# Optimization experiments

Measured on AMD Instinct MI355X. Metric: run time of the kernel, lower is better.

Reference implementation:

```python
import jax, jax.numpy as jnp
import numpy as np

N = 50000      # nodes
E = 800000     # edges
H = 4          # heads (all layers)
D = 64         # per-head out dim (n_hidden == n_classes == 64)
IN = 256       # in_feats; also H*D so identity residual is valid
NEG_SLOPE = 0.2


def setup_inputs() -> dict:
    key = jax.random.key(0)
    ks = jax.random.split(key, 16)
    x = jax.random.normal(ks[0], (N, IN), dtype=jnp.float32)
    src = jax.random.randint(ks[1], (E,), 0, N, dtype=jnp.int32)
    dst = jax.random.randint(ks[2], (E,), 0, N, dtype=jnp.int32)
    inp = {"x": x, "src": src, "dst": dst}
    fan_ins = [IN, H * D, H * D]  # layer input widths
    for i, fin in enumerate(fan_ins):
        s = 1.0 / np.sqrt(fin)
        inp[f"W{i}"] = jax.random.normal(ks[3 + 4 * i], (fin, H * D), dtype=jnp.float32) * s
        inp[f"al{i}"] = jax.random.normal(ks[4 + 4 * i], (H, D), dtype=jnp.float32) * s
        inp[f"ar{i}"] = jax.random.normal(ks[5 + 4 * i], (H, D), dtype=jnp.float32) * s
        inp[f"b{i}"] = jnp.zeros((H * D,), dtype=jnp.float32)
    return inp


def _gat_layer(h, src, dst, W, al, ar, b, residual, activate):
    # project: [N, in] @ [in, H*D] -> [N, H, D]
    feat = (h @ W).reshape(-1, H, D)
    el = jnp.sum(feat * al, axis=-1)            # [N, H]
    er = jnp.sum(feat * ar, axis=-1)            # [N, H]
    e = jax.nn.leaky_relu(el[src] + er[dst], NEG_SLOPE)  # [E, H]
    # edge softmax per destination node (stable: subtract per-dst max)
    emax = jax.ops.segment_max(e, dst, num_segments=N)  # [N, H]
    e = jnp.exp(e - emax[dst])
    denom = jax.ops.segment_sum(e, dst, num_segments=N)  # [N, H]
    alpha = e / denom[dst]                               # [E, H]
    # message + scatter-aggregate: [E, H, D] summed into [N, H, D]
    out = jax.ops.segment_sum(alpha[:, :, None] * feat[src], dst, num_segments=N)
    if residual:
        out = out + h.reshape(-1, H, D)  # identity residual (in == H*D)
    out = out + b.reshape(1, H, D)
    if activate:
        out = jax.nn.elu(out)
    return out


def reference(x, src, dst, W0, al0, ar0, b0, W1, al1, ar1, b1, W2, al2, ar2, b2):
    h = _gat_layer(x, src, dst, W0, al0, ar0, b0, False, True).reshape(N, H * D)
    h = _gat_layer(h, src, dst, W1, al1, ar1, b1, True, True).reshape(N, H * D)
    h = _gat_layer(h, src, dst, W2, al2, ar2, b2, True, False).mean(axis=1)  # [N, D]
    return h
```

## Files before the change

### kernel.cpp

```cpp
#include <hip/hip_runtime.h>
#include <math.h>

#define N_NODES 50000
#define N_EDGES 800000
#define HD 256
#define NHEAD 4
#define DH 64

typedef short bf16x8 __attribute__((ext_vector_type(8)));
typedef float f32x4 __attribute__((ext_vector_type(4)));

__device__ __forceinline__ unsigned short f2bf(float f) {
    unsigned u = __float_as_uint(f);
    return (unsigned short)((u + 0x7fffu + ((u >> 16) & 1u)) >> 16);
}
__device__ __forceinline__ float bf2f(unsigned short h) {
    return __uint_as_float((unsigned)h << 16);
}
__device__ __forceinline__ int origk(int k) {
    return (k & ~63) | ((k & 3) * 16 + ((k >> 2) & 15));
}

__global__ void packw_k(const float* __restrict__ W0, const float* __restrict__ W1,
                        const float* __restrict__ W2, unsigned short* __restrict__ Wp,
                        int* __restrict__ deg) {
    int blk = blockIdx.x;
    int L = blk >> 7, t = blk & 127;
    const float* W = L == 0 ? W0 : L == 1 ? W1 : W2;
    int nt = t >> 3, kt = t & 7;
    int lane = threadIdx.x;
    for (int i = blk * 64 + lane; i < N_NODES; i += 384 * 64) deg[i] = 0;
    int col = nt * 16 + (lane & 15);
    int kb = kt * 32 + (lane >> 4) * 8;
    unsigned short v[8];
#pragma unroll
    for (int j = 0; j < 8; j++) {
        int k = kb + j;
        if (L > 0) k = origk(k);
        v[j] = f2bf(W[(size_t)k * 256 + col]);
    }
    *(bf16x8*)(Wp + ((size_t)(L * 128 + t) * 64 + lane) * 8) = *(bf16x8*)v;
}

__device__ __forceinline__ void mfma_tile(const unsigned short* Asl,
                                          const unsigned short* wbase,
                                          int lane, f32x4 acc[4][4]) {
#pragma unroll
    for (int kk = 0; kk < 8; kk++) {
        bf16x8 a[4], b[4];
#pragma unroll
        for (int m = 0; m < 4; m++) {
            int r = m * 16 + (lane & 15);
            int kb = kk * 32 + (lane >> 4) * 8;
            int byt = (r * 512 + kb * 2) ^ ((r & 7) << 4);
            a[m] = *(const bf16x8*)((const char*)Asl + byt);
        }
#pragma unroll
        for (int n = 0; n < 4; n++)
            b[n] = *(const bf16x8*)(wbase + ((size_t)(n * 8 + kk) * 64 + lane) * 8);
#pragma unroll
        for (int m = 0; m < 4; m++)
#pragma unroll
            for (int n = 0; n < 4; n++)
                acc[m][n] = __builtin_amdgcn_mfma_f32_16x16x32_bf16(a[m], b[n],
                                                                    acc[m][n], 0, 0, 0);
    }
}

__device__ __forceinline__ void epilogue_tile(f32x4 acc[4][4], int bm, int wv, int lane,
                                              const float* __restrict__ al,
                                              const float* __restrict__ ar,
                                              unsigned short* __restrict__ C,
                                              float* __restrict__ el,
                                              float* __restrict__ er, int M) {
    int rr = lane >> 4, cc = lane & 15;
    float alv[4], arv[4];
#pragma unroll
    for (int n = 0; n < 4; n++) {
        alv[n] = al[wv * 64 + n * 16 + cc];
        arv[n] = ar[wv * 64 + n * 16 + cc];
    }
    float vl[16], vr[16];
#pragma unroll
    for (int m = 0; m < 4; m++)
#pragma unroll
        for (int r = 0; r < 4; r++) {
            float ep = 0.f, rp = 0.f;
#pragma unroll
            for (int n = 0; n < 4; n++) {
                ep = fmaf(acc[m][n][r], alv[n], ep);
                rp = fmaf(acc[m][n][r], arv[n], rp);
            }
            vl[m * 4 + r] = ep;
            vr[m * 4 + r] = rp;
        }
    float l8[8], r8[8];
#pragma unroll
    for (int i = 0; i < 8; i++) {
        float xs = (cc & 1) ? vl[2 * i] : vl[2 * i + 1];
        float xk = (cc & 1) ? vl[2 * i + 1] : vl[2 * i];
        l8[i] = xk + __shfl_xor(xs, 1);
        float ys = (cc & 1) ? vr[2 * i] : vr[2 * i + 1];
        float yk = (cc & 1) ? vr[2 * i + 1] : vr[2 * i];
        r8[i] = yk + __shfl_xor(ys, 1);
    }
    float l4[4], r4[4];
#pragma unroll
    for (int i = 0; i < 4; i++) {
        float xs = (cc & 2) ? l8[2 * i] : l8[2 * i + 1];
        float xk = (cc & 2) ? l8[2 * i + 1] : l8[2 * i];
        l4[i] = xk + __shfl_xor(xs, 2);
        float ys = (cc & 2) ? r8[2 * i] : r8[2 * i + 1];
        float yk = (cc & 2) ? r8[2 * i + 1] : r8[2 * i];
        r4[i] = yk + __shfl_xor(ys, 2);
    }
    float l2[2], r2[2];
#pragma unroll
    for (int i = 0; i < 2; i++) {
        float xs = (cc & 4) ? l4[2 * i] : l4[2 * i + 1];
        float xk = (cc & 4) ? l4[2 * i + 1] : l4[2 * i];
        l2[i] = xk + __shfl_xor(xs, 4);
        float ys = (cc & 4) ? r4[2 * i] : r4[2 * i + 1];
        float yk = (cc & 4) ? r4[2 * i + 1] : r4[2 * i];
        r2[i] = yk + __shfl_xor(ys, 4);
    }
    {
        float xs = (cc & 8) ? l2[0] : l2[1];
        float xk = (cc & 8) ? l2[1] : l2[0];
        float lv = xk + __shfl_xor(xs, 8);
        float ys = (cc & 8) ? r2[0] : r2[1];
        float yk = (cc & 8) ? r2[1] : r2[0];
        float rv = yk + __shfl_xor(ys, 8);
        int row_e = bm + (cc >> 2) * 16 + rr * 4 + (cc & 3);
        if (row_e < M) {
            el[(size_t)row_e * NHEAD + wv] = lv;
            er[(size_t)row_e * NHEAD + wv] = rv;
        }
    }
#pragma unroll
    for (int m = 0; m < 4; m++) {
#pragma unroll
        for (int r = 0; r < 4; r++) {
            int row = bm + m * 16 + rr * 4 + r;
            if (row < M) {
                unsigned short p4[4] = {f2bf(acc[m][0][r]), f2bf(acc[m][1][r]),
                                        f2bf(acc[m][2][r]), f2bf(acc[m][3][r])};
                *(ushort4*)(C + (size_t)row * 256 + wv * 64 + cc * 4) = *(ushort4*)p4;
            }
        }
    }
}

__global__ __launch_bounds__(256) void gemm0_k(const float* __restrict__ A,
                                               const unsigned short* __restrict__ Wp,
                                               const float* __restrict__ al,
                                               const float* __restrict__ ar,
                                               unsigned short* __restrict__ C,
                                               float* __restrict__ el,
                                               float* __restrict__ er, int M) {
    __shared__ unsigned short Asl[64 * 256];
    int tid = threadIdx.x, wv = tid >> 6, lane = tid & 63;
    int bm = blockIdx.x * 64;
#pragma unroll
    for (int i = 0; i < 8; i++) {
        int chunk = i * 256 + tid;
        int r = chunk >> 5, kc = (chunk & 31) * 8;
        float4 f0, f1;
        if (bm + r < M) {
            const float* p = A + (size_t)(bm + r) * 256 + kc;
            f0 = *(const float4*)p;
            f1 = *(const float4*)(p + 4);
        } else {
            f0 = f1 = make_float4(0.f, 0.f, 0.f, 0.f);
        }
        unsigned short tmp[8] = {f2bf(f0.x), f2bf(f0.y), f2bf(f0.z), f2bf(f0.w),
                                 f2bf(f1.x), f2bf(f1.y), f2bf(f1.z), f2bf(f1.w)};
        int b = (r * 512 + kc * 2) ^ ((r & 7) << 4);
        *(bf16x8*)((char*)Asl + b) = *(bf16x8*)tmp;
    }
    __syncthreads();
    const unsigned short* wbase = Wp + (size_t)(wv * 4) * 8 * 64 * 8;
    f32x4 acc[4][4] = {};
    mfma_tile(Asl, wbase, lane, acc);
    epilogue_tile(acc, bm, wv, lane, al, ar, C, el, er, M);
}

__global__ __launch_bounds__(256) void gemm2_k(const unsigned short* __restrict__ A,
                                               const unsigned short* __restrict__ Wp,
                                               const float* __restrict__ al,
                                               const float* __restrict__ ar,
                                               unsigned short* __restrict__ C,
                                               float* __restrict__ el,
                                               float* __restrict__ er, int M) {
    __shared__ unsigned short Asl[2][64 * 256];
    int tid = threadIdx.x, wv = tid >> 6, lane = tid & 63;
    int bm0 = blockIdx.x * 128, bm1 = bm0 + 64;
#pragma unroll
    for (int i = 0; i < 8; i++) {
        int chunk = i * 256 + tid;
        int r = chunk >> 5;
        int c16 = (chunk & 31) ^ (r & 7);
        int grow = bm0 + r; if (grow >= M) grow = M - 1;
        __builtin_amdgcn_global_load_lds(
            (const __attribute__((address_space(1))) unsigned int*)
                (A + (size_t)grow * 256 + c16 * 8),
            (__attribute__((address_space(3))) unsigned int*)
                ((char*)Asl[0] + (size_t)chunk * 16),
            16, 0, 0);
    }
#pragma unroll
    for (int i = 0; i < 8; i++) {
        int chunk = i * 256 + tid;
        int r = chunk >> 5;
        int c16 = (chunk & 31) ^ (r & 7);
        int grow = bm1 + r; if (grow >= M) grow = M - 1;
        __builtin_amdgcn_global_load_lds(
            (const __attribute__((address_space(1))) unsigned int*)
                (A + (size_t)grow * 256 + c16 * 8),
            (__attribute__((address_space(3))) unsigned int*)
                ((char*)Asl[1] + (size_t)chunk * 16),
            16, 0, 0);
    }
    asm volatile("s_waitcnt vmcnt(8)" ::: "memory");
    __builtin_amdgcn_sched_barrier(0);
    __builtin_amdgcn_s_barrier();
    const unsigned short* wbase = Wp + (size_t)(wv * 4) * 8 * 64 * 8;
    f32x4 acc[4][4] = {};
    mfma_tile(Asl[0], wbase, lane, acc);
    asm volatile("s_waitcnt vmcnt(0)" ::: "memory");
    __builtin_amdgcn_sched_barrier(0);
    __builtin_amdgcn_s_barrier();
    epilogue_tile(acc, bm0, wv, lane, al, ar, C, el, er, M);
    f32x4 acc2[4][4] = {};
    mfma_tile(Asl[1], wbase, lane, acc2);
    epilogue_tile(acc2, bm1, wv, lane, al, ar, C, el, er, M);
}

__global__ void hist_k(const int* __restrict__ dst, int* __restrict__ deg) {
    int e = (blockIdx.x * 256 + threadIdx.x) * 2;
    if (e + 1 < N_EDGES) {
        int2 d2 = *(const int2*)(dst + e);
        atomicAdd(&deg[d2.x], 1);
        atomicAdd(&deg[d2.y], 1);
    } else if (e < N_EDGES) {
        atomicAdd(&deg[dst[e]], 1);
    }
}

__global__ __launch_bounds__(1024) void scan1_k(const int* __restrict__ deg,
                                                int* __restrict__ rowptr,
                                                int* __restrict__ bsum) {
    __shared__ int wsum[16];
    int tid = threadIdx.x, lane = tid & 63, wv = tid >> 6;
    int i = blockIdx.x * 1024 + tid;
    int v = (i < N_NODES) ? deg[i] : 0;
    int sc = v;
#pragma unroll
    for (int o = 1; o < 64; o <<= 1) {
        int t = __shfl_up(sc, o);
        if (lane >= o) sc += t;
    }
    if (lane == 63) wsum[wv] = sc;
    __syncthreads();
    if (wv == 0 && lane < 16) {
        int ws = wsum[lane];
#pragma unroll
        for (int o = 1; o < 16; o <<= 1) {
            int t = __shfl_up(ws, o);
            if (lane >= o) ws += t;
        }
        wsum[lane] = ws;
    }
    __syncthreads();
    int incl = sc + (wv > 0 ? wsum[wv - 1] : 0);
    if (i < N_NODES) rowptr[i + 1] = incl;
    if (tid == 1023) bsum[blockIdx.x] = incl;
}

__global__ __launch_bounds__(1024) void scan3_k(int* __restrict__ rowptr,
                                                const int* __restrict__ bsum,
                                                int* __restrict__ cursor, int nb) {
    __shared__ int boff_s;
    int tid = threadIdx.x;
    if (tid < 64) {
        int v = (tid < nb) ? bsum[tid] : 0;
        int sc = v;
#pragma unroll
        for (int o = 1; o < 64; o <<= 1) {
            int t = __shfl_up(sc, o);
            if ((tid & 63) >= o) sc += t;
        }
        if (tid == (int)blockIdx.x) boff_s = sc - v;
    }
    __syncthreads();
    int off = boff_s;
    int i = blockIdx.x * 1024 + tid;
    if (blockIdx.x == 0 && tid == 0) { rowptr[0] = 0; cursor[0] = 0; }
    if (i < N_NODES) {
        int v = rowptr[i + 1] + off;
        rowptr[i + 1] = v;
        if (i + 1 < N_NODES) cursor[i + 1] = v;
    }
}

__global__ void scatter_k(const int* __restrict__ src, const int* __restrict__ dst,
                          int* __restrict__ cursor, int* __restrict__ csr_src) {
    int e = (blockIdx.x * 256 + threadIdx.x) * 2;
    if (e + 1 < N_EDGES) {
        int2 s2 = *(const int2*)(src + e);
        int2 d2 = *(const int2*)(dst + e);
        csr_src[atomicAdd(&cursor[d2.x], 1)] = s2.x;
        csr_src[atomicAdd(&cursor[d2.y], 1)] = s2.y;
    } else if (e < N_EDGES) {
        csr_src[atomicAdd(&cursor[dst[e]], 1)] = src[e];
    }
}

template <int MODE>
__global__ __launch_bounds__(256) void agg_k(const int* __restrict__ rowptr,
                                             const int* __restrict__ csr_src,
                                             const float* __restrict__ el,
                                             const float* __restrict__ er,
                                             const unsigned short* __restrict__ feat,
                                             const unsigned short* __restrict__ resid,
                                             const float* __restrict__ bias,
                                             float* __restrict__ out,
                                             unsigned short* __restrict__ hb) {
    __shared__ int   ws_s[4][64];
    __shared__ float ws_w[4][4][68];
    int wv = threadIdx.x >> 6, lane = threadIdx.x & 63;
    int node = blockIdx.x * 4 + wv;
    if (node >= N_NODES) return;
    int beg = rowptr[node], end = rowptr[node + 1];
    float4 er4 = *(const float4*)(er + (size_t)node * 4);
    float4 acc0 = make_float4(0.f, 0.f, 0.f, 0.f);
    float4 acc1 = make_float4(0.f, 0.f, 0.f, 0.f);
    float4 den = make_float4(0.f, 0.f, 0.f, 0.f);
    int h = lane >> 4;
    int l8 = lane * 8;
    const char* fb = (const char*)feat;
    for (int base = beg; base < end; base += 64) {
        int j = base + lane;
        int soff = 0;
        float4 w = make_float4(0.f, 0.f, 0.f, 0.f);
        if (j < end) {
            int s = csr_src[j];
            soff = s << 9;
            float4 l4 = *(const float4*)(el + (size_t)s * 4);
            float vx = l4.x + er4.x; vx = vx > 0.f ? vx : 0.2f * vx;
            float vy = l4.y + er4.y; vy = vy > 0.f ? vy : 0.2f * vy;
            float vz = l4.z + er4.z; vz = vz > 0.f ? vz : 0.2f * vz;
            float vw = l4.w + er4.w; vw = vw > 0.f ? vw : 0.2f * vw;
            w.x = expf(vx); w.y = expf(vy); w.z = expf(vz); w.w = expf(vw);
            den.x += w.x; den.y += w.y; den.z += w.z; den.w += w.w;
        }
        ws_s[wv][lane] = soff;
        ws_w[wv][0][lane] = w.x;
        ws_w[wv][1][lane] = w.y;
        ws_w[wv][2][lane] = w.z;
        ws_w[wv][3][lane] = w.w;
        __builtin_amdgcn_wave_barrier();
        int cnt = end - base; if (cnt > 64) cnt = 64;
        int cnt4 = (cnt + 3) & ~3;
        for (int k = 0; k < cnt4; k += 4) {
            int4   so = *(const int4*)&ws_s[wv][k];
            float4 w4 = *(const float4*)&ws_w[wv][h][k];
            ushort4 u0 = *(const ushort4*)(fb + (so.x + l8));
            ushort4 u1 = *(const ushort4*)(fb + (so.y + l8));
            ushort4 u2 = *(const ushort4*)(fb + (so.z + l8));
            ushort4 u3 = *(const ushort4*)(fb + (so.w + l8));
            acc0.x = fmaf(w4.x, bf2f(u0.x), acc0.x);
            acc0.y = fmaf(w4.x, bf2f(u0.y), acc0.y);
            acc0.z = fmaf(w4.x, bf2f(u0.z), acc0.z);
            acc0.w = fmaf(w4.x, bf2f(u0.w), acc0.w);
            acc1.x = fmaf(w4.y, bf2f(u1.x), acc1.x);
            acc1.y = fmaf(w4.y, bf2f(u1.y), acc1.y);
            acc1.z = fmaf(w4.y, bf2f(u1.z), acc1.z);
            acc1.w = fmaf(w4.y, bf2f(u1.w), acc1.w);
            acc0.x = fmaf(w4.z, bf2f(u2.x), acc0.x);
            acc0.y = fmaf(w4.z, bf2f(u2.y), acc0.y);
            acc0.z = fmaf(w4.z, bf2f(u2.z), acc0.z);
            acc0.w = fmaf(w4.z, bf2f(u2.w), acc0.w);
            acc1.x = fmaf(w4.w, bf2f(u3.x), acc1.x);
            acc1.y = fmaf(w4.w, bf2f(u3.y), acc1.y);
            acc1.z = fmaf(w4.w, bf2f(u3.z), acc1.z);
            acc1.w = fmaf(w4.w, bf2f(u3.w), acc1.w);
        }
        __builtin_amdgcn_wave_barrier();
    }
    float4 acc;
    acc.x = acc0.x + acc1.x; acc.y = acc0.y + acc1.y;
    acc.z = acc0.z + acc1.z; acc.w = acc0.w + acc1.w;
#pragma unroll
    for (int o = 1; o < 64; o <<= 1) {
        den.x += __shfl_xor(den.x, o);
        den.y += __shfl_xor(den.y, o);
        den.z += __shfl_xor(den.z, o);
        den.w += __shfl_xor(den.w, o);
    }
    float den_me = h == 0 ? den.x : h == 1 ? den.y : h == 2 ? den.z : den.w;
    float r = den_me > 0.f ? 1.f / den_me : 0.f;
    int cc = lane & 15;
    float4 b4;
    b4.x = bias[h * 64 + 0 * 16 + cc];
    b4.y = bias[h * 64 + 1 * 16 + cc];
    b4.z = bias[h * 64 + 2 * 16 + cc];
    b4.w = bias[h * 64 + 3 * 16 + cc];
    float4 o4;
    o4.x = acc.x * r + b4.x;
    o4.y = acc.y * r + b4.y;
    o4.z = acc.z * r + b4.z;
    o4.w = acc.w * r + b4.w;
    if (MODE >= 1) {
        ushort4 r4 = *(const ushort4*)(resid + (size_t)node * HD + lane * 4);
        o4.x += bf2f(r4.x); o4.y += bf2f(r4.y);
        o4.z += bf2f(r4.z); o4.w += bf2f(r4.w);
    }
    if (MODE <= 1) {
        o4.x = o4.x > 0.f ? o4.x : expm1f(o4.x);
        o4.y = o4.y > 0.f ? o4.y : expm1f(o4.y);
        o4.z = o4.z > 0.f ? o4.z : expm1f(o4.z);
        o4.w = o4.w > 0.f ? o4.w : expm1f(o4.w);
        ushort4 hv;
        hv.x = f2bf(o4.x); hv.y = f2bf(o4.y); hv.z = f2bf(o4.z); hv.w = f2bf(o4.w);
        *(ushort4*)(hb + (size_t)node * HD + lane * 4) = hv;
    } else {
        o4.x += __shfl_xor(o4.x, 16); o4.x += __shfl_xor(o4.x, 32);
        o4.y += __shfl_xor(o4.y, 16); o4.y += __shfl_xor(o4.y, 32);
        o4.z += __shfl_xor(o4.z, 16); o4.z += __shfl_xor(o4.z, 32);
        o4.w += __shfl_xor(o4.w, 16); o4.w += __shfl_xor(o4.w, 32);
        if (lane < 16) {
            float* po = out + (size_t)node * DH;
            po[0 * 16 + lane] = o4.x * 0.25f;
            po[1 * 16 + lane] = o4.y * 0.25f;
            po[2 * 16 + lane] = o4.z * 0.25f;
            po[3 * 16 + lane] = o4.w * 0.25f;
        }
    }
}

extern "C" void kernel_launch(void* const* d_in, const int* in_sizes, int n_in,
                              void* d_out, int out_size, void* d_ws, size_t ws_size,
                              hipStream_t stream) {
    const float* x   = (const float*)d_in[0];
    const int*   src = (const int*)d_in[1];
    const int*   dst = (const int*)d_in[2];
    const float* W[3]  = {(const float*)d_in[3], (const float*)d_in[7],  (const float*)d_in[11]};
    const float* al[3] = {(const float*)d_in[4], (const float*)d_in[8],  (const float*)d_in[12]};
    const float* ar[3] = {(const float*)d_in[5], (const float*)d_in[9],  (const float*)d_in[13]};
    const float* bb[3] = {(const float*)d_in[6], (const float*)d_in[10], (const float*)d_in[14]};

    size_t big = (size_t)N_NODES * HD;
    unsigned short* featb = (unsigned short*)d_ws;
    unsigned short* hb1 = featb + big;
    unsigned short* hb2 = hb1 + big;
    float* el = (float*)(hb2 + big);
    float* er = el + (size_t)N_NODES * NHEAD;
    int* deg     = (int*)(er + (size_t)N_NODES * NHEAD);
    int* rowptr  = deg + 50048;
    int* cursor  = rowptr + 50048;
    int* csr_src = cursor + 50048;
    int* bsum    = csr_src + N_EDGES;
    unsigned short* Wp = (unsigned short*)(bsum + 64);

    const int NB = (N_NODES + 1023) / 1024;

    packw_k<<<384, 64, 0, stream>>>(W[0], W[1], W[2], Wp, deg);
    hist_k<<<(N_EDGES / 2 + 255) / 256, 256, 0, stream>>>(dst, deg);
    scan1_k<<<NB, 1024, 0, stream>>>(deg, rowptr, bsum);
    scan3_k<<<NB, 1024, 0, stream>>>(rowptr, bsum, cursor, NB);
    scatter_k<<<(N_EDGES / 2 + 255) / 256, 256, 0, stream>>>(src, dst, cursor, csr_src);

    int g0grid = (N_NODES + 63) / 64;
    int g2grid = (N_NODES + 127) / 128;
    int agrid = (N_NODES + 3) / 4;

    gemm0_k<<<g0grid, 256, 0, stream>>>(x, Wp, al[0], ar[0], featb, el, er, N_NODES);
    agg_k<0><<<agrid, 256, 0, stream>>>(rowptr, csr_src, el, er, featb,
                                        nullptr, bb[0], nullptr, hb1);
    gemm2_k<<<g2grid, 256, 0, stream>>>(hb1, Wp + (size_t)1 * 128 * 64 * 8,
                                        al[1], ar[1], featb, el, er, N_NODES);
    agg_k<1><<<agrid, 256, 0, stream>>>(rowptr, csr_src, el, er, featb,
                                        hb1, bb[1], nullptr, hb2);
    gemm2_k<<<g2grid, 256, 0, stream>>>(hb2, Wp + (size_t)2 * 128 * 64 * 8,
                                        al[2], ar[2], featb, el, er, N_NODES);
    agg_k<2><<<agrid, 256, 0, stream>>>(rowptr, csr_src, el, er, featb,
                                        hb2, bb[2], (float*)d_out, nullptr);
}
```

Measured before the change: 340.0 us.

## Store el in bf16 and split degree histogram into four sub-histograms

Stores the per-node source attention logits (el) as bf16 instead of fp32. This halves the size of the random gather of el done in the aggregation kernels. Separately, the degree histogram is spread across four interleaved copies selected by thread index, which cuts atomic contention; scan1 sums the four copies when it reads them. The cost is lower precision in the attention logits and a larger buffer to zero.

```diff
diff --git a/kernel.cpp b/kernel.cpp
--- a/kernel.cpp
+++ b/kernel.cpp
@@ -6,6 +6,7 @@
 #define HD 256
 #define NHEAD 4
 #define DH 64
+#define NPAD 50048
 
 typedef short bf16x8 __attribute__((ext_vector_type(8)));
 typedef float f32x4 __attribute__((ext_vector_type(4)));
@@ -29,7 +30,7 @@
     const float* W = L == 0 ? W0 : L == 1 ? W1 : W2;
     int nt = t >> 3, kt = t & 7;
     int lane = threadIdx.x;
-    for (int i = blk * 64 + lane; i < N_NODES; i += 384 * 64) deg[i] = 0;
+    for (int i = blk * 64 + lane; i < 4 * NPAD; i += 384 * 64) deg[i] = 0;
     int col = nt * 16 + (lane & 15);
     int kb = kt * 32 + (lane >> 4) * 8;
     unsigned short v[8];
@@ -71,7 +72,7 @@
                                               const float* __restrict__ al,
                                               const float* __restrict__ ar,
                                               unsigned short* __restrict__ C,
-                                              float* __restrict__ el,
+                                              unsigned short* __restrict__ el,
                                               float* __restrict__ er, int M) {
     int rr = lane >> 4, cc = lane & 15;
     float alv[4], arv[4];
@@ -133,7 +134,7 @@
         float rv = yk + __shfl_xor(ys, 8);
         int row_e = bm + (cc >> 2) * 16 + rr * 4 + (cc & 3);
         if (row_e < M) {
-            el[(size_t)row_e * NHEAD + wv] = lv;
+            el[(size_t)row_e * NHEAD + wv] = f2bf(lv);
             er[(size_t)row_e * NHEAD + wv] = rv;
         }
     }
@@ -156,7 +157,7 @@
                                                const float* __restrict__ al,
                                                const float* __restrict__ ar,
                                                unsigned short* __restrict__ C,
-                                               float* __restrict__ el,
+                                               unsigned short* __restrict__ el,
                                                float* __restrict__ er, int M) {
     __shared__ unsigned short Asl[64 * 256];
     int tid = threadIdx.x, wv = tid >> 6, lane = tid & 63;
@@ -190,7 +191,7 @@
                                                const float* __restrict__ al,
                                                const float* __restrict__ ar,
                                                unsigned short* __restrict__ C,
-                                               float* __restrict__ el,
+                                               unsigned short* __restrict__ el,
                                                float* __restrict__ er, int M) {
     __shared__ unsigned short Asl[2][64 * 256];
     int tid = threadIdx.x, wv = tid >> 6, lane = tid & 63;
@@ -237,13 +238,15 @@
 }
 
 __global__ void hist_k(const int* __restrict__ dst, int* __restrict__ deg) {
-    int e = (blockIdx.x * 256 + threadIdx.x) * 2;
+    int t = blockIdx.x * 256 + threadIdx.x;
+    int e = t * 2;
+    int* mydeg = deg + (size_t)(threadIdx.x & 3) * NPAD;
     if (e + 1 < N_EDGES) {
         int2 d2 = *(const int2*)(dst + e);
-        atomicAdd(&deg[d2.x], 1);
-        atomicAdd(&deg[d2.y], 1);
+        atomicAdd(&mydeg[d2.x], 1);
+        atomicAdd(&mydeg[d2.y], 1);
     } else if (e < N_EDGES) {
-        atomicAdd(&deg[dst[e]], 1);
+        atomicAdd(&mydeg[dst[e]], 1);
     }
 }
 
@@ -253,7 +256,9 @@
     __shared__ int wsum[16];
     int tid = threadIdx.x, lane = tid & 63, wv = tid >> 6;
     int i = blockIdx.x * 1024 + tid;
-    int v = (i < N_NODES) ? deg[i] : 0;
+    int v = 0;
+    if (i < N_NODES)
+        v = deg[i] + deg[i + NPAD] + deg[i + 2 * NPAD] + deg[i + 3 * NPAD];
     int sc = v;
 #pragma unroll
     for (int o = 1; o < 64; o <<= 1) {
@@ -319,7 +324,7 @@
 template <int MODE>
 __global__ __launch_bounds__(256) void agg_k(const int* __restrict__ rowptr,
                                              const int* __restrict__ csr_src,
-                                             const float* __restrict__ el,
+                                             const unsigned short* __restrict__ el,
                                              const float* __restrict__ er,
                                              const unsigned short* __restrict__ feat,
                                              const unsigned short* __restrict__ resid,
@@ -346,11 +351,11 @@
         if (j < end) {
             int s = csr_src[j];
             soff = s << 9;
-            float4 l4 = *(const float4*)(el + (size_t)s * 4);
-            float vx = l4.x + er4.x; vx = vx > 0.f ? vx : 0.2f * vx;
-            float vy = l4.y + er4.y; vy = vy > 0.f ? vy : 0.2f * vy;
-            float vz = l4.z + er4.z; vz = vz > 0.f ? vz : 0.2f * vz;
-            float vw = l4.w + er4.w; vw = vw > 0.f ? vw : 0.2f * vw;
+            ushort4 l4u = *(const ushort4*)(el + (size_t)s * 4);
+            float vx = bf2f(l4u.x) + er4.x; vx = vx > 0.f ? vx : 0.2f * vx;
+            float vy = bf2f(l4u.y) + er4.y; vy = vy > 0.f ? vy : 0.2f * vy;
+            float vz = bf2f(l4u.z) + er4.z; vz = vz > 0.f ? vz : 0.2f * vz;
+            float vw = bf2f(l4u.w) + er4.w; vw = vw > 0.f ? vw : 0.2f * vw;
             w.x = expf(vx); w.y = expf(vy); w.z = expf(vz); w.w = expf(vw);
             den.x += w.x; den.y += w.y; den.z += w.z; den.w += w.w;
         }
@@ -454,12 +459,12 @@
     unsigned short* featb = (unsigned short*)d_ws;
     unsigned short* hb1 = featb + big;
     unsigned short* hb2 = hb1 + big;
-    float* el = (float*)(hb2 + big);
-    float* er = el + (size_t)N_NODES * NHEAD;
-    int* deg     = (int*)(er + (size_t)N_NODES * NHEAD);
-    int* rowptr  = deg + 50048;
-    int* cursor  = rowptr + 50048;
-    int* csr_src = cursor + 50048;
+    unsigned short* el = hb2 + big;
+    float* er = (float*)(el + (size_t)NPAD * NHEAD);
+    int* deg     = (int*)(er + (size_t)NPAD * NHEAD);
+    int* rowptr  = deg + 4 * NPAD;
+    int* cursor  = rowptr + NPAD;
+    int* csr_src = cursor + NPAD;
     int* bsum    = csr_src + N_EDGES;
     unsigned short* Wp = (unsigned short*)(bsum + 64);
 
```

Result: faster. 327.1 us (-3.8%).
